# Kernel tuning notes

Hardware: AMD Instinct MI355X
Metric: run time of the kernel (lower is better)

Reference implementation:

```python
import jax, jax.numpy as jnp
import numpy as np

N_NODES = 100000
N_EDGES = 1600000
IN, HID, OUT = 128, 128, 64


def setup_inputs() -> dict:
    key = jax.random.key(0)
    ks = jax.random.split(key, 6)
    x = jax.random.normal(ks[0], (N_NODES, IN), dtype=jnp.float32)
    W1 = jax.random.normal(ks[1], (IN, HID), dtype=jnp.float32) * (1.0 / np.sqrt(IN))
    b1 = jnp.zeros((HID,), dtype=jnp.float32)
    W2 = jax.random.normal(ks[2], (HID, OUT), dtype=jnp.float32) * (1.0 / np.sqrt(HID))
    b2 = jnp.zeros((OUT,), dtype=jnp.float32)
    edge_src = jax.random.randint(ks[3], (N_EDGES,), 0, N_NODES, dtype=jnp.int32)
    edge_dst = jax.random.randint(ks[4], (N_EDGES,), 0, N_NODES, dtype=jnp.int32)
    return {"x": x, "W1": W1, "b1": b1, "W2": W2, "b2": b2,
            "edge_src": edge_src, "edge_dst": edge_dst}


def reference(x, W1, b1, W2, b2, edge_src, edge_dst):
    N = x.shape[0]
    # in-degree per dst node (DGL 'gcn' aggregator normalizer)
    deg = jax.ops.segment_sum(jnp.ones_like(edge_dst, dtype=x.dtype), edge_dst,
                              num_segments=N)  # [N]
    inv = 1.0 / (deg + 1.0)  # [N]

    def sage_gcn(h, W, b):
        # sum over in-neighbors, add self, mean-normalize, then linear
        agg = jax.ops.segment_sum(h[edge_src], edge_dst, num_segments=N)  # [N, d]
        h_neigh = (agg + h) * inv[:, None]
        return h_neigh @ W + b

    h = jax.nn.relu(sage_gcn(x, W1, b1))
    # dropout is identity here (eval mode / deterministic reference)
    return sage_gcn(h, W2, b2)
```

## Files before the change

### kernel.cpp

```cpp
#include <hip/hip_runtime.h>

#define NN 100000
#define NE 1600000
#define NBUC 782
#define NBLKA 256
#define CHA 6250
#define LG (NBUC * NBLKA)

__device__ __forceinline__ unsigned short f2bf(float f) {
    unsigned int u = __float_as_uint(f);
    u += 0x7FFFu + ((u >> 16) & 1u);
    return (unsigned short)(u >> 16);
}
__device__ __forceinline__ float bf_lo(unsigned int u) { return __uint_as_float(u << 16); }
__device__ __forceinline__ float bf_hi(unsigned int u) { return __uint_as_float(u & 0xFFFF0000u); }

__global__ void binA_kernel(const int* __restrict__ dst, int* __restrict__ G, int E) {
    __shared__ int hist[NBUC];
    int t = threadIdx.x;
    for (int i = t; i < NBUC; i += 256) hist[i] = 0;
    __syncthreads();
    int s0 = blockIdx.x * CHA;
    int s1 = min(E, s0 + CHA);
    for (int i = s0 + t; i < s1; i += 256) atomicAdd(&hist[dst[i] >> 7], 1);
    __syncthreads();
    for (int i = t; i < NBUC; i += 256) G[i * NBLKA + blockIdx.x] = hist[i];
}

__global__ void gsum_kernel(const int* __restrict__ G, int* __restrict__ gb) {
    __shared__ int s[512];
    int t = threadIdx.x;
    s[t] = G[blockIdx.x * 512 + t];
    __syncthreads();
    for (int o = 256; o > 0; o >>= 1) {
        if (t < o) s[t] += s[t + o];
        __syncthreads();
    }
    if (t == 0) gb[blockIdx.x] = s[0];
}

__global__ void scanb_kernel(int* __restrict__ bsum, int nb) {
    __shared__ int s[512];
    int t = threadIdx.x;
    s[t] = (t < nb) ? bsum[t] : 0;
    __syncthreads();
    for (int o = 1; o < 512; o <<= 1) {
        int v = (t >= o) ? s[t - o] : 0;
        __syncthreads();
        if (t >= o) s[t] += v;
        __syncthreads();
    }
    if (t < nb) bsum[t] = (t == 0) ? 0 : s[t - 1];
}

__global__ void gscan_kernel(int* __restrict__ G, const int* __restrict__ gb) {
    __shared__ int s[512];
    int t = threadIdx.x;
    int i = blockIdx.x * 512 + t;
    int v = G[i];
    s[t] = v;
    __syncthreads();
    for (int o = 1; o < 512; o <<= 1) {
        int u = (t >= o) ? s[t - o] : 0;
        __syncthreads();
        if (t >= o) s[t] += u;
        __syncthreads();
    }
    G[i] = gb[blockIdx.x] + s[t] - v;
}

__global__ void binB_kernel(const int* __restrict__ src, const int* __restrict__ dst,
                            const int* __restrict__ G, unsigned long long* __restrict__ ebuf,
                            int E) {
    __shared__ int cur[NBUC];
    int t = threadIdx.x;
    for (int i = t; i < NBUC; i += 256) cur[i] = G[i * NBLKA + blockIdx.x];
    __syncthreads();
    int s0 = blockIdx.x * CHA;
    int s1 = min(E, s0 + CHA);
    for (int i = s0 + t; i < s1; i += 256) {
        int d = dst[i];
        int b = d >> 7;
        int pos = atomicAdd(&cur[b], 1);
        ebuf[pos] = ((unsigned long long)(unsigned int)d << 32) | (unsigned int)src[i];
    }
}

__global__ void fillC_kernel(const unsigned long long* __restrict__ ebuf,
                             const int* __restrict__ G, int* __restrict__ rowptr,
                             float* __restrict__ inv, int* __restrict__ col, int E, int N) {
    __shared__ int cnt[128];
    __shared__ int sc[128];
    int b = blockIdx.x;
    int t = threadIdx.x;
    int segStart = G[b * NBLKA];
    int segEnd = (b + 1 < NBUC) ? G[(b + 1) * NBLKA] : E;
    int nodeBase = b << 7;

    if (t < 128) cnt[t] = 0;
    __syncthreads();
    for (int i = segStart + t; i < segEnd; i += 256) {
        int d = (int)(ebuf[i] >> 32);
        atomicAdd(&cnt[d - nodeBase], 1);
    }
    __syncthreads();
    if (t < 128) sc[t] = cnt[t];
    __syncthreads();
    for (int o = 1; o < 128; o <<= 1) {
        int v = 0;
        if (t < 128 && t >= o) v = sc[t - o];
        __syncthreads();
        if (t < 128 && t >= o) sc[t] += v;
        __syncthreads();
    }
    if (t < 128) {
        int excl = (t == 0) ? 0 : sc[t - 1];
        int n = nodeBase + t;
        if (n < N) {
            rowptr[n] = segStart + excl;
            inv[n] = 1.0f / (float)(cnt[t] + 1);
        }
        sc[t] = segStart + excl;
    }
    if (b == 0 && t == 0) rowptr[N] = E;
    __syncthreads();
    for (int i = segStart + t; i < segEnd; i += 256) {
        unsigned long long p = ebuf[i];
        int d = (int)(p >> 32);
        int s = (int)(p & 0xFFFFFFFFull);
        int pos = atomicAdd(&sc[d - nodeBase], 1);
        col[pos] = s;
    }
}

__global__ void gemm1_kernel(const float* __restrict__ x, const float* __restrict__ W1,
                             unsigned short* __restrict__ ybf, int N) {
    __shared__ float xs[8][128];
    const int j = threadIdx.x;
    const int nb = blockIdx.x * 8;

    #pragma unroll
    for (int m = 0; m < 8; ++m) xs[m][j] = x[(size_t)(nb + m) * 128 + j];
    __syncthreads();

    float acc[8];
    #pragma unroll
    for (int m = 0; m < 8; ++m) acc[m] = 0.0f;

    #pragma unroll 4
    for (int k = 0; k < 128; k += 4) {
        float w0 = W1[(k + 0) * 128 + j];
        float w1 = W1[(k + 1) * 128 + j];
        float w2 = W1[(k + 2) * 128 + j];
        float w3 = W1[(k + 3) * 128 + j];
        #pragma unroll
        for (int m = 0; m < 8; ++m) {
            float4 v = *reinterpret_cast<const float4*>(&xs[m][k]);
            acc[m] = fmaf(v.x, w0, acc[m]);
            acc[m] = fmaf(v.y, w1, acc[m]);
            acc[m] = fmaf(v.z, w2, acc[m]);
            acc[m] = fmaf(v.w, w3, acc[m]);
        }
    }

    #pragma unroll
    for (int m = 0; m < 8; ++m) ybf[(size_t)(nb + m) * 128 + j] = f2bf(acc[m]);
}

__global__ void gemm2_kernel(const float* __restrict__ h1, const float* __restrict__ W2,
                             unsigned short* __restrict__ zbf, int N) {
    __shared__ float hs[32][128];
    const int t = threadIdx.x;
    const int j = t & 63;
    const int grp = t >> 6;
    const int nb = blockIdx.x * 32;

    for (int i = t; i < 32 * 128; i += 256) {
        hs[i >> 7][i & 127] = h1[(size_t)nb * 128 + i];
    }
    __syncthreads();

    float acc[8];
    #pragma unroll
    for (int m = 0; m < 8; ++m) acc[m] = 0.0f;

    #pragma unroll 4
    for (int k = 0; k < 128; k += 4) {
        float w0 = W2[(k + 0) * 64 + j];
        float w1 = W2[(k + 1) * 64 + j];
        float w2 = W2[(k + 2) * 64 + j];
        float w3 = W2[(k + 3) * 64 + j];
        #pragma unroll
        for (int m = 0; m < 8; ++m) {
            float4 v = *reinterpret_cast<const float4*>(&hs[grp * 8 + m][k]);
            acc[m] = fmaf(v.x, w0, acc[m]);
            acc[m] = fmaf(v.y, w1, acc[m]);
            acc[m] = fmaf(v.z, w2, acc[m]);
            acc[m] = fmaf(v.w, w3, acc[m]);
        }
    }

    #pragma unroll
    for (int m = 0; m < 8; ++m) {
        zbf[(size_t)(nb + grp * 8 + m) * 64 + j] = f2bf(acc[m]);
    }
}

__global__ void agg1_kernel(const unsigned short* __restrict__ ybf,
                            const int* __restrict__ rowptr, const int* __restrict__ col,
                            const float* __restrict__ inv, const float* __restrict__ b1,
                            float* __restrict__ h1, int N) {
    int wave = (blockIdx.x * blockDim.x + threadIdx.x) >> 6;
    if (wave >= N) return;
    int lane = threadIdx.x & 63;
    int start = rowptr[wave], end = rowptr[wave + 1];
    const unsigned int* yb = (const unsigned int*)ybf;

    float ax0 = 0, ay0 = 0, ax1 = 0, ay1 = 0, ax2 = 0, ay2 = 0, ax3 = 0, ay3 = 0;
    int e = start;
    for (; e + 3 < end; e += 4) {
        int s0 = __builtin_amdgcn_readfirstlane(col[e]);
        int s1 = __builtin_amdgcn_readfirstlane(col[e + 1]);
        int s2 = __builtin_amdgcn_readfirstlane(col[e + 2]);
        int s3 = __builtin_amdgcn_readfirstlane(col[e + 3]);
        unsigned int u0 = yb[(size_t)s0 * 64 + lane];
        unsigned int u1 = yb[(size_t)s1 * 64 + lane];
        unsigned int u2 = yb[(size_t)s2 * 64 + lane];
        unsigned int u3 = yb[(size_t)s3 * 64 + lane];
        ax0 += bf_lo(u0); ay0 += bf_hi(u0);
        ax1 += bf_lo(u1); ay1 += bf_hi(u1);
        ax2 += bf_lo(u2); ay2 += bf_hi(u2);
        ax3 += bf_lo(u3); ay3 += bf_hi(u3);
    }
    for (; e < end; ++e) {
        int s0 = __builtin_amdgcn_readfirstlane(col[e]);
        unsigned int u0 = yb[(size_t)s0 * 64 + lane];
        ax0 += bf_lo(u0); ay0 += bf_hi(u0);
    }
    float sx = (ax0 + ax1) + (ax2 + ax3);
    float sy = (ay0 + ay1) + (ay2 + ay3);

    unsigned int us = yb[(size_t)wave * 64 + lane];
    float2 bb = *reinterpret_cast<const float2*>(b1 + lane * 2);
    float iv = inv[wave];
    float2 r;
    r.x = fmaxf(fmaf(sx + bf_lo(us), iv, bb.x), 0.0f);
    r.y = fmaxf(fmaf(sy + bf_hi(us), iv, bb.y), 0.0f);
    *reinterpret_cast<float2*>(h1 + (size_t)wave * 128 + lane * 2) = r;
}

__global__ void agg2_kernel(const unsigned short* __restrict__ zbf,
                            const int* __restrict__ rowptr, const int* __restrict__ col,
                            const float* __restrict__ inv, const float* __restrict__ b2,
                            float* __restrict__ out, int N) {
    int node = (blockIdx.x * blockDim.x + threadIdx.x) >> 5;
    if (node >= N) return;
    int lane = threadIdx.x & 31;
    int start = rowptr[node], end = rowptr[node + 1];
    const unsigned int* zb = (const unsigned int*)zbf;

    float ax0 = 0, ay0 = 0, ax1 = 0, ay1 = 0, ax2 = 0, ay2 = 0, ax3 = 0, ay3 = 0;
    int e = start;
    for (; e + 3 < end; e += 4) {
        int s0 = col[e], s1 = col[e + 1], s2 = col[e + 2], s3 = col[e + 3];
        unsigned int u0 = zb[(size_t)s0 * 32 + lane];
        unsigned int u1 = zb[(size_t)s1 * 32 + lane];
        unsigned int u2 = zb[(size_t)s2 * 32 + lane];
        unsigned int u3 = zb[(size_t)s3 * 32 + lane];
        ax0 += bf_lo(u0); ay0 += bf_hi(u0);
        ax1 += bf_lo(u1); ay1 += bf_hi(u1);
        ax2 += bf_lo(u2); ay2 += bf_hi(u2);
        ax3 += bf_lo(u3); ay3 += bf_hi(u3);
    }
    for (; e < end; ++e) {
        unsigned int u0 = zb[(size_t)col[e] * 32 + lane];
        ax0 += bf_lo(u0); ay0 += bf_hi(u0);
    }
    float sx = (ax0 + ax1) + (ax2 + ax3);
    float sy = (ay0 + ay1) + (ay2 + ay3);

    unsigned int us = zb[(size_t)node * 32 + lane];
    float2 bb = *reinterpret_cast<const float2*>(b2 + lane * 2);
    float iv = inv[node];
    float2 r;
    r.x = fmaf(sx + bf_lo(us), iv, bb.x);
    r.y = fmaf(sy + bf_hi(us), iv, bb.y);
    *reinterpret_cast<float2*>(out + (size_t)node * 64 + lane * 2) = r;
}

extern "C" void kernel_launch(void* const* d_in, const int* in_sizes, int n_in,
                              void* d_out, int out_size, void* d_ws, size_t ws_size,
                              hipStream_t stream) {
    const float* x   = (const float*)d_in[0];
    const float* W1  = (const float*)d_in[1];
    const float* b1  = (const float*)d_in[2];
    const float* W2  = (const float*)d_in[3];
    const float* b2  = (const float*)d_in[4];
    const int* esrc  = (const int*)d_in[5];
    const int* edst  = (const int*)d_in[6];
    float* out = (float*)d_out;

    unsigned long long* ebuf = (unsigned long long*)d_ws;
    int*   G      = (int*)(ebuf + NE);
    int*   gb     = G + LG;
    int*   rowptr = gb + 512;
    int*   col    = rowptr + NN + 1;
    float* inv    = (float*)(col + NE);
    unsigned short* ybf = (unsigned short*)(inv + NN);
    unsigned short* zbf = ybf + (size_t)NN * 128;
    float* h1     = (float*)(zbf + (size_t)NN * 64);

    binA_kernel<<<NBLKA, 256, 0, stream>>>(edst, G, NE);
    gsum_kernel<<<LG / 512, 512, 0, stream>>>(G, gb);
    scanb_kernel<<<1, 512, 0, stream>>>(gb, LG / 512);
    gscan_kernel<<<LG / 512, 512, 0, stream>>>(G, gb);
    binB_kernel<<<NBLKA, 256, 0, stream>>>(esrc, edst, G, ebuf, NE);
    fillC_kernel<<<NBUC, 256, 0, stream>>>(ebuf, G, rowptr, inv, col, NE, NN);

    gemm1_kernel<<<NN / 8, 128, 0, stream>>>(x, W1, ybf, NN);
    agg1_kernel<<<NN / 4, 256, 0, stream>>>(ybf, rowptr, col, inv, b1, h1, NN);

    gemm2_kernel<<<(NN + 31) / 32, 256, 0, stream>>>(h1, W2, zbf, NN);
    agg2_kernel<<<NN / 8, 256, 0, stream>>>(zbf, rowptr, col, inv, b2, out, NN);
}
```

Before: 422.3 us.

## Replace FP32 FMA GEMMs with split-bf16 MFMA GEMMs

Both dense GEMMs now run on MFMA 16x16x32 bf16 instructions instead of scalar fp32 FMA loops. Inputs, weights and the hidden activations are each split into high and low bf16 parts, and three MFMAs per tile approximate fp32 accuracy. This needs extra conversion kernels and separate high/low buffers, with rows padded to a multiple of 64. The workspace is re-laid out so ybf aliases ebuf and h1 reuses the x buffers. The aim is to remove the ALU-bound fp32 GEMM cost at the price of extra conversion passes and more memory traffic.

```diff
diff --git a/kernel.cpp b/kernel.cpp
--- a/kernel.cpp
+++ b/kernel.cpp
@@ -1,19 +1,58 @@
 #include <hip/hip_runtime.h>
 
 #define NN 100000
+#define NNP 100032
 #define NE 1600000
 #define NBUC 782
 #define NBLKA 256
 #define CHA 6250
 #define LG (NBUC * NBLKA)
 
+typedef __attribute__((ext_vector_type(8))) short short8;
+typedef __attribute__((ext_vector_type(4))) float f32x4;
+
 __device__ __forceinline__ unsigned short f2bf(float f) {
     unsigned int u = __float_as_uint(f);
     u += 0x7FFFu + ((u >> 16) & 1u);
     return (unsigned short)(u >> 16);
 }
+__device__ __forceinline__ float ubf(unsigned short h) {
+    return __uint_as_float((unsigned int)h << 16);
+}
 __device__ __forceinline__ float bf_lo(unsigned int u) { return __uint_as_float(u << 16); }
 __device__ __forceinline__ float bf_hi(unsigned int u) { return __uint_as_float(u & 0xFFFF0000u); }
+
+__global__ void convx_kernel(const float* __restrict__ x, unsigned short* __restrict__ xh,
+                             unsigned short* __restrict__ xl) {
+    int t = blockIdx.x * 256 + threadIdx.x;
+    float4 v = reinterpret_cast<const float4*>(x)[t];
+    ushort4 h, l;
+    h.x = f2bf(v.x); l.x = f2bf(v.x - ubf(h.x));
+    h.y = f2bf(v.y); l.y = f2bf(v.y - ubf(h.y));
+    h.z = f2bf(v.z); l.z = f2bf(v.z - ubf(h.z));
+    h.w = f2bf(v.w); l.w = f2bf(v.w - ubf(h.w));
+    reinterpret_cast<ushort4*>(xh)[t] = h;
+    reinterpret_cast<ushort4*>(xl)[t] = l;
+}
+
+__global__ void convw_kernel(const float* __restrict__ W1, const float* __restrict__ W2,
+                             unsigned short* __restrict__ w1th, unsigned short* __restrict__ w1tl,
+                             unsigned short* __restrict__ w2th, unsigned short* __restrict__ w2tl) {
+    int n = blockIdx.x;
+    int k = threadIdx.x;
+    if (n < 128) {
+        float w = W1[k * 128 + n];
+        unsigned short h = f2bf(w);
+        w1th[n * 128 + k] = h;
+        w1tl[n * 128 + k] = f2bf(w - ubf(h));
+    } else {
+        int n2 = n - 128;
+        float w = W2[k * 64 + n2];
+        unsigned short h = f2bf(w);
+        w2th[n2 * 128 + k] = h;
+        w2tl[n2 * 128 + k] = f2bf(w - ubf(h));
+    }
+}
 
 __global__ void binA_kernel(const int* __restrict__ dst, int* __restrict__ G, int E) {
     __shared__ int hist[NBUC];
@@ -133,83 +172,97 @@
     }
 }
 
-__global__ void gemm1_kernel(const float* __restrict__ x, const float* __restrict__ W1,
-                             unsigned short* __restrict__ ybf, int N) {
-    __shared__ float xs[8][128];
-    const int j = threadIdx.x;
-    const int nb = blockIdx.x * 8;
-
-    #pragma unroll
-    for (int m = 0; m < 8; ++m) xs[m][j] = x[(size_t)(nb + m) * 128 + j];
-    __syncthreads();
-
-    float acc[8];
-    #pragma unroll
-    for (int m = 0; m < 8; ++m) acc[m] = 0.0f;
-
-    #pragma unroll 4
-    for (int k = 0; k < 128; k += 4) {
-        float w0 = W1[(k + 0) * 128 + j];
-        float w1 = W1[(k + 1) * 128 + j];
-        float w2 = W1[(k + 2) * 128 + j];
-        float w3 = W1[(k + 3) * 128 + j];
+__global__ __launch_bounds__(256) void gemm1m_kernel(
+    const unsigned short* __restrict__ xh, const unsigned short* __restrict__ xl,
+    const unsigned short* __restrict__ w1th, const unsigned short* __restrict__ w1tl,
+    unsigned short* __restrict__ ybf) {
+    const int wid = threadIdx.x >> 6;
+    const int lane = threadIdx.x & 63;
+    const int rbase = blockIdx.x * 64 + wid * 16;
+    const int r = lane & 15;
+    const int kg = lane >> 4;
+
+    f32x4 acc[8];
+    #pragma unroll
+    for (int j = 0; j < 8; ++j) acc[j] = (f32x4){0.0f, 0.0f, 0.0f, 0.0f};
+
+    const short* xhp = (const short*)xh;
+    const short* xlp = (const short*)xl;
+    const short* wh  = (const short*)w1th;
+    const short* wl  = (const short*)w1tl;
+
+    #pragma unroll
+    for (int kk = 0; kk < 4; ++kk) {
+        const int ko = kk * 32 + kg * 8;
+        short8 a_h = *reinterpret_cast<const short8*>(xhp + (size_t)(rbase + r) * 128 + ko);
+        short8 a_l = *reinterpret_cast<const short8*>(xlp + (size_t)(rbase + r) * 128 + ko);
         #pragma unroll
-        for (int m = 0; m < 8; ++m) {
-            float4 v = *reinterpret_cast<const float4*>(&xs[m][k]);
-            acc[m] = fmaf(v.x, w0, acc[m]);
-            acc[m] = fmaf(v.y, w1, acc[m]);
-            acc[m] = fmaf(v.z, w2, acc[m]);
-            acc[m] = fmaf(v.w, w3, acc[m]);
+        for (int j = 0; j < 8; ++j) {
+            short8 b_h = *reinterpret_cast<const short8*>(wh + (j * 16 + r) * 128 + ko);
+            short8 b_l = *reinterpret_cast<const short8*>(wl + (j * 16 + r) * 128 + ko);
+            acc[j] = __builtin_amdgcn_mfma_f32_16x16x32_bf16(a_h, b_h, acc[j], 0, 0, 0);
+            acc[j] = __builtin_amdgcn_mfma_f32_16x16x32_bf16(a_h, b_l, acc[j], 0, 0, 0);
+            acc[j] = __builtin_amdgcn_mfma_f32_16x16x32_bf16(a_l, b_h, acc[j], 0, 0, 0);
         }
     }
 
     #pragma unroll
-    for (int m = 0; m < 8; ++m) ybf[(size_t)(nb + m) * 128 + j] = f2bf(acc[m]);
-}
-
-__global__ void gemm2_kernel(const float* __restrict__ h1, const float* __restrict__ W2,
-                             unsigned short* __restrict__ zbf, int N) {
-    __shared__ float hs[32][128];
-    const int t = threadIdx.x;
-    const int j = t & 63;
-    const int grp = t >> 6;
-    const int nb = blockIdx.x * 32;
-
-    for (int i = t; i < 32 * 128; i += 256) {
-        hs[i >> 7][i & 127] = h1[(size_t)nb * 128 + i];
-    }
-    __syncthreads();
-
-    float acc[8];
-    #pragma unroll
-    for (int m = 0; m < 8; ++m) acc[m] = 0.0f;
-
-    #pragma unroll 4
-    for (int k = 0; k < 128; k += 4) {
-        float w0 = W2[(k + 0) * 64 + j];
-        float w1 = W2[(k + 1) * 64 + j];
-        float w2 = W2[(k + 2) * 64 + j];
-        float w3 = W2[(k + 3) * 64 + j];
+    for (int j = 0; j < 8; ++j) {
         #pragma unroll
-        for (int m = 0; m < 8; ++m) {
-            float4 v = *reinterpret_cast<const float4*>(&hs[grp * 8 + m][k]);
-            acc[m] = fmaf(v.x, w0, acc[m]);
-            acc[m] = fmaf(v.y, w1, acc[m]);
-            acc[m] = fmaf(v.z, w2, acc[m]);
-            acc[m] = fmaf(v.w, w3, acc[m]);
+        for (int q = 0; q < 4; ++q) {
+            ybf[(size_t)(rbase + kg * 4 + q) * 128 + j * 16 + r] = f2bf(acc[j][q]);
         }
     }
-
-    #pragma unroll
-    for (int m = 0; m < 8; ++m) {
-        zbf[(size_t)(nb + grp * 8 + m) * 64 + j] = f2bf(acc[m]);
+}
+
+__global__ __launch_bounds__(256) void gemm2m_kernel(
+    const unsigned short* __restrict__ h1h, const unsigned short* __restrict__ h1l,
+    const unsigned short* __restrict__ w2th, const unsigned short* __restrict__ w2tl,
+    unsigned short* __restrict__ zbf) {
+    const int wid = threadIdx.x >> 6;
+    const int lane = threadIdx.x & 63;
+    const int rbase = blockIdx.x * 64 + wid * 16;
+    const int r = lane & 15;
+    const int kg = lane >> 4;
+
+    f32x4 acc[4];
+    #pragma unroll
+    for (int j = 0; j < 4; ++j) acc[j] = (f32x4){0.0f, 0.0f, 0.0f, 0.0f};
+
+    const short* hhp = (const short*)h1h;
+    const short* hlp = (const short*)h1l;
+    const short* wh  = (const short*)w2th;
+    const short* wl  = (const short*)w2tl;
+
+    #pragma unroll
+    for (int kk = 0; kk < 4; ++kk) {
+        const int ko = kk * 32 + kg * 8;
+        short8 a_h = *reinterpret_cast<const short8*>(hhp + (size_t)(rbase + r) * 128 + ko);
+        short8 a_l = *reinterpret_cast<const short8*>(hlp + (size_t)(rbase + r) * 128 + ko);
+        #pragma unroll
+        for (int j = 0; j < 4; ++j) {
+            short8 b_h = *reinterpret_cast<const short8*>(wh + (j * 16 + r) * 128 + ko);
+            short8 b_l = *reinterpret_cast<const short8*>(wl + (j * 16 + r) * 128 + ko);
+            acc[j] = __builtin_amdgcn_mfma_f32_16x16x32_bf16(a_h, b_h, acc[j], 0, 0, 0);
+            acc[j] = __builtin_amdgcn_mfma_f32_16x16x32_bf16(a_h, b_l, acc[j], 0, 0, 0);
+            acc[j] = __builtin_amdgcn_mfma_f32_16x16x32_bf16(a_l, b_h, acc[j], 0, 0, 0);
+        }
+    }
+
+    #pragma unroll
+    for (int j = 0; j < 4; ++j) {
+        #pragma unroll
+        for (int q = 0; q < 4; ++q) {
+            zbf[(size_t)(rbase + kg * 4 + q) * 64 + j * 16 + r] = f2bf(acc[j][q]);
+        }
     }
 }
 
 __global__ void agg1_kernel(const unsigned short* __restrict__ ybf,
                             const int* __restrict__ rowptr, const int* __restrict__ col,
                             const float* __restrict__ inv, const float* __restrict__ b1,
-                            float* __restrict__ h1, int N) {
+                            unsigned short* __restrict__ h1h, unsigned short* __restrict__ h1l,
+                            int N) {
     int wave = (blockIdx.x * blockDim.x + threadIdx.x) >> 6;
     if (wave >= N) return;
     int lane = threadIdx.x & 63;
@@ -243,10 +296,14 @@
     unsigned int us = yb[(size_t)wave * 64 + lane];
     float2 bb = *reinterpret_cast<const float2*>(b1 + lane * 2);
     float iv = inv[wave];
-    float2 r;
-    r.x = fmaxf(fmaf(sx + bf_lo(us), iv, bb.x), 0.0f);
-    r.y = fmaxf(fmaf(sy + bf_hi(us), iv, bb.y), 0.0f);
-    *reinterpret_cast<float2*>(h1 + (size_t)wave * 128 + lane * 2) = r;
+    float rx = fmaxf(fmaf(sx + bf_lo(us), iv, bb.x), 0.0f);
+    float ry = fmaxf(fmaf(sy + bf_hi(us), iv, bb.y), 0.0f);
+
+    ushort2 h, l;
+    h.x = f2bf(rx); l.x = f2bf(rx - ubf(h.x));
+    h.y = f2bf(ry); l.y = f2bf(ry - ubf(h.y));
+    *reinterpret_cast<ushort2*>(h1h + (size_t)wave * 128 + lane * 2) = h;
+    *reinterpret_cast<ushort2*>(h1l + (size_t)wave * 128 + lane * 2) = l;
 }
 
 __global__ void agg2_kernel(const unsigned short* __restrict__ zbf,
@@ -300,15 +357,33 @@
     const int* edst  = (const int*)d_in[6];
     float* out = (float*)d_out;
 
-    unsigned long long* ebuf = (unsigned long long*)d_ws;
-    int*   G      = (int*)(ebuf + NE);
-    int*   gb     = G + LG;
-    int*   rowptr = gb + 512;
-    int*   col    = rowptr + NN + 1;
-    float* inv    = (float*)(col + NE);
-    unsigned short* ybf = (unsigned short*)(inv + NN);
-    unsigned short* zbf = ybf + (size_t)NN * 128;
-    float* h1     = (float*)(zbf + (size_t)NN * 64);
+    char* p = (char*)d_ws;
+    unsigned short* ybf = (unsigned short*)p;
+    unsigned long long* ebuf = (unsigned long long*)p;
+    p += (size_t)NNP * 128 * 2;
+    int* G = (int*)p;        p += (size_t)LG * 4;
+    int* gb = (int*)p;       p += 512 * 4;
+    int* rowptr = (int*)p;   p += (size_t)(NN + 4) * 4;
+    int* col = (int*)p;      p += (size_t)NE * 4;
+    float* inv = (float*)p;  p += (size_t)NN * 4;
+    unsigned short* w1th = (unsigned short*)p; p += 128 * 128 * 2;
+    unsigned short* w1tl = (unsigned short*)p; p += 128 * 128 * 2;
+    unsigned short* w2th = (unsigned short*)p; p += 64 * 128 * 2;
+    unsigned short* w2tl = (unsigned short*)p; p += 64 * 128 * 2;
+    unsigned short* xh = (unsigned short*)p;   p += (size_t)NNP * 128 * 2;
+    unsigned short* xl = (unsigned short*)p;   p += (size_t)NNP * 128 * 2;
+    unsigned short* zbf = (unsigned short*)p;  p += (size_t)NNP * 64 * 2;
+    unsigned short* h1h = xh;
+    unsigned short* h1l = xl;
+
+    size_t padOff = (size_t)NN * 128 * 2;
+    size_t padBytes = (size_t)(NNP - NN) * 128 * 2;
+    hipMemsetAsync(xh + (size_t)NN * 128, 0, padBytes, stream);
+    hipMemsetAsync(xl + (size_t)NN * 128, 0, padBytes, stream);
+    (void)padOff;
+
+    convx_kernel<<<NN * 32 / 256, 256, 0, stream>>>(x, xh, xl);
+    convw_kernel<<<192, 128, 0, stream>>>(W1, W2, w1th, w1tl, w2th, w2tl);
 
     binA_kernel<<<NBLKA, 256, 0, stream>>>(edst, G, NE);
     gsum_kernel<<<LG / 512, 512, 0, stream>>>(G, gb);
@@ -317,9 +392,10 @@
     binB_kernel<<<NBLKA, 256, 0, stream>>>(esrc, edst, G, ebuf, NE);
     fillC_kernel<<<NBUC, 256, 0, stream>>>(ebuf, G, rowptr, inv, col, NE, NN);
 
-    gemm1_kernel<<<NN / 8, 128, 0, stream>>>(x, W1, ybf, NN);
-    agg1_kernel<<<NN / 4, 256, 0, stream>>>(ybf, rowptr, col, inv, b1, h1, NN);
-
-    gemm2_kernel<<<(NN + 31) / 32, 256, 0, stream>>>(h1, W2, zbf, NN);
+    gemm1m_kernel<<<NNP / 64, 256, 0, stream>>>(xh, xl, w1th, w1tl, ybf);
+    agg1_kernel<<<NN / 4, 256, 0, stream>>>(ybf, rowptr, col, inv, b1, h1h, h1l, NN);
+
+
+    gemm2m_kernel<<<NNP / 64, 256, 0, stream>>>(h1h, h1l, w2th, w2tl, zbf);
     agg2_kernel<<<NN / 8, 256, 0, stream>>>(zbf, rowptr, col, inv, b2, out, NN);
 }
```

New measurement: 419.0 us. No clear change (-0.8%).
